# Kernel optimization log

Measured on AMD Instinct MI355X. Metric: run time of the kernel, lower is better.

The kernel has to match this reference:

```python
import jax, jax.numpy as jnp
import numpy as np
import math

D_MODEL = 1024
N_HEADS = 16
HEAD_DIM = D_MODEL // N_HEADS
SEQ_LEN = 8192
INCLUDE_LOCAL = 2


def get_dilated_positions(seq_len, include_local=2):
    # Faithful numpy port of the torch pattern generator (runs once at setup).
    max_attend = include_local + int(math.ceil(math.log2(seq_len + 1)))
    positions = np.zeros((seq_len, max_attend), dtype=np.int64)
    mask = np.zeros((seq_len, max_attend), dtype=bool)
    for i in range(seq_len):
        ap = [i]
        for j in range(1, include_local + 1):
            if i - j >= 0:
                ap.append(i - j)
        k = 2
        while i - 2 ** k >= 0:
            ap.append(i - 2 ** k)
            k += 1
        positions[i, :len(ap)] = ap
        mask[i, :len(ap)] = True
    return positions, mask


def setup_inputs() -> dict:
    key = jax.random.key(0)
    kx, kq, kk, kv, ko = jax.random.split(key, 5)
    x = jax.random.normal(kx, (1, SEQ_LEN, D_MODEL), dtype=jnp.float32)
    # nn.Linear(bias=False) weights, torch layout [out_features, in_features]
    s = 0.02
    q_w = jax.random.normal(kq, (D_MODEL, D_MODEL), dtype=jnp.float32) * s
    k_w = jax.random.normal(kk, (D_MODEL, D_MODEL), dtype=jnp.float32) * s
    v_w = jax.random.normal(kv, (D_MODEL, D_MODEL), dtype=jnp.float32) * s
    o_w = jax.random.normal(ko, (D_MODEL, D_MODEL), dtype=jnp.float32) * s
    pos_np, mask_np = get_dilated_positions(SEQ_LEN, INCLUDE_LOCAL)
    return {
        "x": x,
        "q_w": q_w, "k_w": k_w, "v_w": v_w, "o_w": o_w,
        "positions": jnp.asarray(pos_np),   # (S, A) int64 indices
        "attend_mask": jnp.asarray(mask_np) # (S, A) bool
    }


def reference(x, q_w, k_w, v_w, o_w, positions, attend_mask):
    B, S, _ = x.shape
    H, Dh = N_HEADS, HEAD_DIM
    scale = Dh ** -0.5

    q = (x @ q_w.T).reshape(B, S, H, Dh).transpose(0, 2, 1, 3)  # (B,H,S,Dh)
    k = (x @ k_w.T).reshape(B, S, H, Dh).transpose(0, 2, 1, 3)
    v = (x @ v_w.T).reshape(B, S, H, Dh).transpose(0, 2, 1, 3)

    # Gather K/V at the dilated positions: (B,H,S,A,Dh)
    k_sparse = k[:, :, positions, :]
    v_sparse = v[:, :, positions, :]

    scores = jnp.einsum('bhsd,bhsad->bhsa', q, k_sparse) * scale
    scores = jnp.where(attend_mask[None, None, :, :], scores, -jnp.inf)
    attn = jax.nn.softmax(scores, axis=-1)  # dropout p in eval / 0.0 -> identity

    out = jnp.einsum('bhsa,bhsad->bhsd', attn, v_sparse)
    out = out.transpose(0, 2, 1, 3).reshape(B, S, D_MODEL)
    return out @ o_w.T
```

## Files before the change

kernel.cpp:

```cpp
#include <hip/hip_runtime.h>
#include <hip/hip_bf16.h>

typedef __bf16 bf16_t;
typedef __bf16 bf16x4 __attribute__((ext_vector_type(4)));
typedef __bf16 bf16x8 __attribute__((ext_vector_type(8)));
typedef float floatx16 __attribute__((ext_vector_type(16)));

#define SEQ    8192
#define DM     1024
#define NHEADS 16
#define HDIM   64

__device__ __forceinline__ void async_ld16(bf16_t* lds, const bf16_t* g) {
  __builtin_amdgcn_global_load_lds(
      (__attribute__((address_space(1))) void*)g,
      (__attribute__((address_space(3))) void*)lds, 16, 0, 0);
}

__global__ __launch_bounds__(256)
void cvt_all(const float* __restrict__ x,  const float* __restrict__ qw,
             const float* __restrict__ kw, const float* __restrict__ vw,
             const float* __restrict__ ow,
             bf16_t* __restrict__ Xb,  bf16_t* __restrict__ QWb,
             bf16_t* __restrict__ KWb, bf16_t* __restrict__ VWb,
             bf16_t* __restrict__ OWb) {
  const int b = blockIdx.x;
  const float* in; bf16_t* out; int g;
  if (b < 8192) { in = x; out = Xb; g = b; }
  else {
    const int w  = (b - 8192) >> 10;
    const int wb = (b - 8192) & 1023;
    switch (w) {
      case 0:  in = qw; out = QWb; break;
      case 1:  in = kw; out = KWb; break;
      case 2:  in = vw; out = VWb; break;
      default: in = ow; out = OWb; break;
    }
    g = wb;
  }
  const int idx = (g * 256 + threadIdx.x) * 4;
  float4 v = *(const float4*)(in + idx);
  bf16x4 o = { (bf16_t)v.x, (bf16_t)v.y, (bf16_t)v.z, (bf16_t)v.w };
  *(bf16x4*)(out + idx) = o;
}

__global__ __launch_bounds__(256)
void gemm_qkv(const bf16_t* __restrict__ A,
              const bf16_t* __restrict__ Bq, const bf16_t* __restrict__ Bk,
              const bf16_t* __restrict__ Bv,
              bf16_t* __restrict__ Cq, bf16_t* __restrict__ Ck, bf16_t* __restrict__ Cv)
{
  const bf16_t* B = (blockIdx.z == 0) ? Bq : (blockIdx.z == 1) ? Bk : Bv;
  bf16_t*       C = (blockIdx.z == 0) ? Cq : (blockIdx.z == 1) ? Ck : Cv;
  constexpr int Kdim = DM;
  __shared__ __attribute__((aligned(16))) bf16_t sA[128 * 64];
  __shared__ __attribute__((aligned(16))) bf16_t sB[128 * 64];

  const int tid  = threadIdx.x;
  const int wave = tid >> 6;
  const int lane = tid & 63;
  const int l31  = lane & 31;
  const int half = lane >> 5;
  const int wr   = (wave >> 1) * 64;
  const int wc   = (wave & 1) * 64;

  const int gc = (lane & 7) ^ ((lane >> 3) & 7);
  const size_t arow0 = (size_t)blockIdx.x * 128 + wave * 32 + (lane >> 3);
  const size_t brow0 = (size_t)blockIdx.y * 128 + wave * 32 + (lane >> 3);
  const bf16_t* Ag = A + arow0 * Kdim + gc * 8;
  const bf16_t* Bg = B + brow0 * Kdim + gc * 8;
  bf16_t* sAw = sA + wave * 32 * 64;
  bf16_t* sBw = sB + wave * 32 * 64;

  floatx16 acc[2][2];
  #pragma unroll
  for (int i = 0; i < 2; ++i)
    #pragma unroll
    for (int j = 0; j < 2; ++j)
      acc[i][j] = (floatx16)(0.0f);

  const int sw = l31 & 7;

  for (int ko = 0; ko < Kdim; ko += 64) {
    #pragma unroll
    for (int n = 0; n < 4; ++n) {
      async_ld16(sAw + n * 512, Ag + (size_t)n * 8 * Kdim + ko);
      async_ld16(sBw + n * 512, Bg + (size_t)n * 8 * Kdim + ko);
    }
    __syncthreads();

    #pragma unroll
    for (int s = 0; s < 4; ++s) {
      const int ck   = s * 2 + half;
      const int slot = (ck ^ sw) * 8;
      bf16x8 af[2], bfr[2];
      #pragma unroll
      for (int mi = 0; mi < 2; ++mi)
        af[mi] = *(const bf16x8*)&sA[(wr + mi * 32 + l31) * 64 + slot];
      #pragma unroll
      for (int ni = 0; ni < 2; ++ni)
        bfr[ni] = *(const bf16x8*)&sB[(wc + ni * 32 + l31) * 64 + slot];

      #pragma unroll
      for (int mi = 0; mi < 2; ++mi)
        #pragma unroll
        for (int ni = 0; ni < 2; ++ni)
          acc[mi][ni] = __builtin_amdgcn_mfma_f32_32x32x16_bf16(af[mi], bfr[ni], acc[mi][ni], 0, 0, 0);
    }

    __syncthreads();
  }

  const float scl = (blockIdx.z == 0) ? 0.125f : 1.0f;
  const int crow0 = blockIdx.x * 128 + wr + 4 * half;
  const int ccol0 = blockIdx.y * 128 + wc + l31;
  #pragma unroll
  for (int mi = 0; mi < 2; ++mi)
    #pragma unroll
    for (int ni = 0; ni < 2; ++ni)
      #pragma unroll
      for (int r = 0; r < 16; ++r) {
        const int row = crow0 + mi * 32 + (r & 3) + 8 * (r >> 2);
        C[(size_t)row * DM + (ccol0 + ni * 32)] = (bf16_t)(acc[mi][ni][r] * scl);
      }
}

__global__ __launch_bounds__(256)
void gemm_out(const bf16_t* __restrict__ A, const bf16_t* __restrict__ B,
              float* __restrict__ C)
{
  constexpr int Kdim = DM;
  __shared__ __attribute__((aligned(16))) bf16_t sA[128 * 64];
  __shared__ __attribute__((aligned(16))) bf16_t sB[128 * 64];

  const int tid  = threadIdx.x;
  const int wave = tid >> 6;
  const int lane = tid & 63;
  const int l31  = lane & 31;
  const int half = lane >> 5;
  const int wr   = (wave >> 1) * 64;
  const int wc   = (wave & 1) * 64;

  const int gc = (lane & 7) ^ ((lane >> 3) & 7);
  const size_t arow0 = (size_t)blockIdx.x * 128 + wave * 32 + (lane >> 3);
  const size_t brow0 = (size_t)blockIdx.y * 128 + wave * 32 + (lane >> 3);
  const bf16_t* Ag = A + arow0 * Kdim + gc * 8;
  const bf16_t* Bg = B + brow0 * Kdim + gc * 8;
  bf16_t* sAw = sA + wave * 32 * 64;
  bf16_t* sBw = sB + wave * 32 * 64;

  floatx16 acc[2][2];
  #pragma unroll
  for (int i = 0; i < 2; ++i)
    #pragma unroll
    for (int j = 0; j < 2; ++j)
      acc[i][j] = (floatx16)(0.0f);

  const int sw = l31 & 7;

  for (int ko = 0; ko < Kdim; ko += 64) {
    #pragma unroll
    for (int n = 0; n < 4; ++n) {
      async_ld16(sAw + n * 512, Ag + (size_t)n * 8 * Kdim + ko);
      async_ld16(sBw + n * 512, Bg + (size_t)n * 8 * Kdim + ko);
    }
    __syncthreads();

    #pragma unroll
    for (int s = 0; s < 4; ++s) {
      const int ck   = s * 2 + half;
      const int slot = (ck ^ sw) * 8;
      bf16x8 af[2], bfr[2];
      #pragma unroll
      for (int mi = 0; mi < 2; ++mi)
        af[mi] = *(const bf16x8*)&sA[(wr + mi * 32 + l31) * 64 + slot];
      #pragma unroll
      for (int ni = 0; ni < 2; ++ni)
        bfr[ni] = *(const bf16x8*)&sB[(wc + ni * 32 + l31) * 64 + slot];

      #pragma unroll
      for (int mi = 0; mi < 2; ++mi)
        #pragma unroll
        for (int ni = 0; ni < 2; ++ni)
          acc[mi][ni] = __builtin_amdgcn_mfma_f32_32x32x16_bf16(af[mi], bfr[ni], acc[mi][ni], 0, 0, 0);
    }

    __syncthreads();
  }

  const int crow0 = blockIdx.x * 128 + wr + 4 * half;
  const int ccol0 = blockIdx.y * 128 + wc + l31;
  #pragma unroll
  for (int mi = 0; mi < 2; ++mi)
    #pragma unroll
    for (int ni = 0; ni < 2; ++ni)
      #pragma unroll
      for (int r = 0; r < 16; ++r) {
        const int row = crow0 + mi * 32 + (r & 3) + 8 * (r >> 2);
        C[(size_t)row * DM + (ccol0 + ni * 32)] = acc[mi][ni][r];
      }
}

__global__ __launch_bounds__(256)
void dilated_attn(const bf16_t* __restrict__ Q, const bf16_t* __restrict__ K,
                  const bf16_t* __restrict__ V, bf16_t* O)
{
  __shared__ float sM[2][64];
  __shared__ float sL[2][64];
  __shared__ float sAcc[2][64][17];

  const int lane = threadIdx.x & 63;
  const int wv   = threadIdx.x >> 6;
  const int ql   = wv >> 1;
  const int sub  = wv & 1;
  const int qb   = (blockIdx.x & 7) * 512 + (blockIdx.x >> 3);
  const int i    = qb * 2 + ql;
  const size_t base = (size_t)i * DM + lane * 16;

  bf16x8 q0 = *(const bf16x8*)(Q + base);
  bf16x8 q1 = *(const bf16x8*)(Q + base + 8);
  float qf[16];
  #pragma unroll
  for (int j = 0; j < 8; ++j) { qf[j] = (float)q0[j]; qf[j + 8] = (float)q1[j]; }

  const int npos = (i == 0) ? 1 : (33 - __builtin_clz((unsigned)i));
  auto pos_addr = [&](int t) -> size_t {
    const int off = (t == 0) ? 0 : (1 << (t - 1));
    return (size_t)(i - off) * DM + lane * 16;
  };

  float m = -INFINITY, l = 0.0f;
  float acc[16];
  #pragma unroll
  for (int j = 0; j < 16; ++j) acc[j] = 0.0f;

  int t = sub;
  if (t < npos) {
    size_t a = pos_addr(t);
    bf16x8 k0 = *(const bf16x8*)(K + a), k1 = *(const bf16x8*)(K + a + 8);
    bf16x8 v0 = *(const bf16x8*)(V + a), v1 = *(const bf16x8*)(V + a + 8);
    while (true) {
      const int tn = t + 2;
      const bool more = (tn < npos);
      bf16x8 nk0, nk1, nv0, nv1;
      if (more) {
        const size_t na = pos_addr(tn);
        nk0 = *(const bf16x8*)(K + na); nk1 = *(const bf16x8*)(K + na + 8);
        nv0 = *(const bf16x8*)(V + na); nv1 = *(const bf16x8*)(V + na + 8);
      }

      float sc = 0.0f;
      #pragma unroll
      for (int j = 0; j < 8; ++j) sc += qf[j] * (float)k0[j] + qf[j + 8] * (float)k1[j];
      sc += __shfl_xor(sc, 1, 64);
      sc += __shfl_xor(sc, 2, 64);

      float mn = fmaxf(m, sc);
      float co = __expf(m - mn);
      float w  = __expf(sc - mn);
      l = l * co + w;
      m = mn;
      #pragma unroll
      for (int j = 0; j < 8; ++j) {
        acc[j]     = acc[j]     * co + w * (float)v0[j];
        acc[j + 8] = acc[j + 8] * co + w * (float)v1[j];
      }

      if (!more) break;
      k0 = nk0; k1 = nk1; v0 = nv0; v1 = nv1;
      t = tn;
    }
  }

  if (sub == 1) {
    sM[ql][lane] = m;
    sL[ql][lane] = l;
    #pragma unroll
    for (int j = 0; j < 16; ++j) sAcc[ql][lane][j] = acc[j];
  }
  __syncthreads();
  if (sub == 0) {
    const float mb = sM[ql][lane], lb = sL[ql][lane];
    const float mt = fmaxf(m, mb);
    const float ca = __expf(m - mt);
    const float cb = __expf(mb - mt);
    const float inv = 1.0f / (l * ca + lb * cb);
    bf16x8 o0, o1;
    #pragma unroll
    for (int j = 0; j < 8; ++j) {
      o0[j] = (bf16_t)((acc[j]     * ca + sAcc[ql][lane][j]     * cb) * inv);
      o1[j] = (bf16_t)((acc[j + 8] * ca + sAcc[ql][lane][j + 8] * cb) * inv);
    }
    *(bf16x8*)(O + base)     = o0;
    *(bf16x8*)(O + base + 8) = o1;
  }
}

extern "C" void kernel_launch(void* const* d_in, const int* in_sizes, int n_in,
                              void* d_out, int out_size, void* d_ws, size_t ws_size,
                              hipStream_t stream) {
  (void)in_sizes; (void)n_in; (void)out_size; (void)ws_size;
  const float* x  = (const float*)d_in[0];
  const float* qw = (const float*)d_in[1];
  const float* kw = (const float*)d_in[2];
  const float* vw = (const float*)d_in[3];
  const float* ow = (const float*)d_in[4];
  float* out = (float*)d_out;

  bf16_t* Xb  = (bf16_t*)d_ws;
  bf16_t* Qb  = Xb  + (size_t)SEQ * DM;
  bf16_t* Kb  = Qb  + (size_t)SEQ * DM;
  bf16_t* Vb  = Kb  + (size_t)SEQ * DM;
  bf16_t* QWb = Vb  + (size_t)SEQ * DM;
  bf16_t* KWb = QWb + (size_t)DM * DM;
  bf16_t* VWb = KWb + (size_t)DM * DM;
  bf16_t* OWb = VWb + (size_t)DM * DM;
  bf16_t* AO  = Qb;

  cvt_all<<<dim3(8192 + 4096), dim3(256), 0, stream>>>(x, qw, kw, vw, ow,
                                                       Xb, QWb, KWb, VWb, OWb);

  gemm_qkv<<<dim3(SEQ / 128, DM / 128, 3), dim3(256), 0, stream>>>(Xb, QWb, KWb, VWb, Qb, Kb, Vb);
  dilated_attn<<<dim3(SEQ / 2), dim3(256), 0, stream>>>(Qb, Kb, Vb, AO);
  gemm_out<<<dim3(SEQ / 128, DM / 128), dim3(256), 0, stream>>>(AO, OWb, out);
}
```

Measured before the change: 213.7 us.

## Double-buffer projection GEMM, split QKV launches, and simplify attention to one wave per query

The QKV projection GEMM gains double-buffered LDS staging, so async global-to-LDS loads of the next K tile overlap MFMA work on the current one. The single fused QKV launch with a blockIdx.z select becomes three separate launches. The attention kernel now gives each wave one full query instead of splitting positions across two waves, which removes the LDS merge and the __syncthreads. The cost is twice the LDS per GEMM block, which may lower occupancy, extra launch overhead, and longer serial per-wave loops in attention.

```diff
diff --git a/kernel.cpp b/kernel.cpp
--- a/kernel.cpp
+++ b/kernel.cpp
@@ -44,17 +44,14 @@
   *(bf16x4*)(out + idx) = o;
 }
 
+
 __global__ __launch_bounds__(256)
-void gemm_qkv(const bf16_t* __restrict__ A,
-              const bf16_t* __restrict__ Bq, const bf16_t* __restrict__ Bk,
-              const bf16_t* __restrict__ Bv,
-              bf16_t* __restrict__ Cq, bf16_t* __restrict__ Ck, bf16_t* __restrict__ Cv)
+void gemm_proj(const bf16_t* __restrict__ A, const bf16_t* __restrict__ B,
+               bf16_t* __restrict__ C, float scl)
 {
-  const bf16_t* B = (blockIdx.z == 0) ? Bq : (blockIdx.z == 1) ? Bk : Bv;
-  bf16_t*       C = (blockIdx.z == 0) ? Cq : (blockIdx.z == 1) ? Ck : Cv;
   constexpr int Kdim = DM;
-  __shared__ __attribute__((aligned(16))) bf16_t sA[128 * 64];
-  __shared__ __attribute__((aligned(16))) bf16_t sB[128 * 64];
+  __shared__ __attribute__((aligned(16))) bf16_t sA[2][128 * 64];
+  __shared__ __attribute__((aligned(16))) bf16_t sB[2][128 * 64];
 
   const int tid  = threadIdx.x;
   const int wave = tid >> 6;
@@ -69,8 +66,6 @@
   const size_t brow0 = (size_t)blockIdx.y * 128 + wave * 32 + (lane >> 3);
   const bf16_t* Ag = A + arow0 * Kdim + gc * 8;
   const bf16_t* Bg = B + brow0 * Kdim + gc * 8;
-  bf16_t* sAw = sA + wave * 32 * 64;
-  bf16_t* sBw = sB + wave * 32 * 64;
 
   floatx16 acc[2][2];
   #pragma unroll
@@ -81,14 +76,14 @@
 
   const int sw = l31 & 7;
 
-  for (int ko = 0; ko < Kdim; ko += 64) {
+  auto stage = [&](int buf, int ko) {
     #pragma unroll
     for (int n = 0; n < 4; ++n) {
-      async_ld16(sAw + n * 512, Ag + (size_t)n * 8 * Kdim + ko);
-      async_ld16(sBw + n * 512, Bg + (size_t)n * 8 * Kdim + ko);
-    }
-    __syncthreads();
-
+      async_ld16(&sA[buf][(wave * 32 + n * 8) * 64], Ag + (size_t)n * 8 * Kdim + ko);
+      async_ld16(&sB[buf][(wave * 32 + n * 8) * 64], Bg + (size_t)n * 8 * Kdim + ko);
+    }
+  };
+  auto compute = [&](int buf) {
     #pragma unroll
     for (int s = 0; s < 4; ++s) {
       const int ck   = s * 2 + half;
@@ -96,22 +91,30 @@
       bf16x8 af[2], bfr[2];
       #pragma unroll
       for (int mi = 0; mi < 2; ++mi)
-        af[mi] = *(const bf16x8*)&sA[(wr + mi * 32 + l31) * 64 + slot];
+        af[mi] = *(const bf16x8*)&sA[buf][(wr + mi * 32 + l31) * 64 + slot];
       #pragma unroll
       for (int ni = 0; ni < 2; ++ni)
-        bfr[ni] = *(const bf16x8*)&sB[(wc + ni * 32 + l31) * 64 + slot];
-
+        bfr[ni] = *(const bf16x8*)&sB[buf][(wc + ni * 32 + l31) * 64 + slot];
       #pragma unroll
       for (int mi = 0; mi < 2; ++mi)
         #pragma unroll
         for (int ni = 0; ni < 2; ++ni)
           acc[mi][ni] = __builtin_amdgcn_mfma_f32_32x32x16_bf16(af[mi], bfr[ni], acc[mi][ni], 0, 0, 0);
     }
-
+  };
+
+  stage(0, 0);
+  __syncthreads();
+  for (int kp = 0; kp < 8; ++kp) {
+    const int ko = kp * 128;
+    stage(1, ko + 64);
+    compute(0);
     __syncthreads();
-  }
-
-  const float scl = (blockIdx.z == 0) ? 0.125f : 1.0f;
+    if (ko + 128 < Kdim) stage(0, ko + 128);
+    compute(1);
+    __syncthreads();
+  }
+
   const int crow0 = blockIdx.x * 128 + wr + 4 * half;
   const int ccol0 = blockIdx.y * 128 + wc + l31;
   #pragma unroll
@@ -126,8 +129,8 @@
 }
 
 __global__ __launch_bounds__(256)
-void gemm_out(const bf16_t* __restrict__ A, const bf16_t* __restrict__ B,
-              float* __restrict__ C)
+void gemm_outk(const bf16_t* __restrict__ A, const bf16_t* __restrict__ B,
+               float* __restrict__ C)
 {
   constexpr int Kdim = DM;
   __shared__ __attribute__((aligned(16))) bf16_t sA[128 * 64];
@@ -205,16 +208,10 @@
 void dilated_attn(const bf16_t* __restrict__ Q, const bf16_t* __restrict__ K,
                   const bf16_t* __restrict__ V, bf16_t* O)
 {
-  __shared__ float sM[2][64];
-  __shared__ float sL[2][64];
-  __shared__ float sAcc[2][64][17];
-
   const int lane = threadIdx.x & 63;
   const int wv   = threadIdx.x >> 6;
-  const int ql   = wv >> 1;
-  const int sub  = wv & 1;
-  const int qb   = (blockIdx.x & 7) * 512 + (blockIdx.x >> 3);
-  const int i    = qb * 2 + ql;
+  const int bid  = blockIdx.x;
+  const int i    = ((bid & 7) * 256 + (bid >> 3)) * 4 + wv;
   const size_t base = (size_t)i * DM + lane * 16;
 
   bf16x8 q0 = *(const bf16x8*)(Q + base);
@@ -234,13 +231,13 @@
   #pragma unroll
   for (int j = 0; j < 16; ++j) acc[j] = 0.0f;
 
-  int t = sub;
-  if (t < npos) {
-    size_t a = pos_addr(t);
+  {
+    size_t a = base;
     bf16x8 k0 = *(const bf16x8*)(K + a), k1 = *(const bf16x8*)(K + a + 8);
     bf16x8 v0 = *(const bf16x8*)(V + a), v1 = *(const bf16x8*)(V + a + 8);
+    int t = 0;
     while (true) {
-      const int tn = t + 2;
+      const int tn = t + 1;
       const bool more = (tn < npos);
       bf16x8 nk0, nk1, nv0, nv1;
       if (more) {
@@ -272,28 +269,15 @@
     }
   }
 
-  if (sub == 1) {
-    sM[ql][lane] = m;
-    sL[ql][lane] = l;
-    #pragma unroll
-    for (int j = 0; j < 16; ++j) sAcc[ql][lane][j] = acc[j];
-  }
-  __syncthreads();
-  if (sub == 0) {
-    const float mb = sM[ql][lane], lb = sL[ql][lane];
-    const float mt = fmaxf(m, mb);
-    const float ca = __expf(m - mt);
-    const float cb = __expf(mb - mt);
-    const float inv = 1.0f / (l * ca + lb * cb);
-    bf16x8 o0, o1;
-    #pragma unroll
-    for (int j = 0; j < 8; ++j) {
-      o0[j] = (bf16_t)((acc[j]     * ca + sAcc[ql][lane][j]     * cb) * inv);
-      o1[j] = (bf16_t)((acc[j + 8] * ca + sAcc[ql][lane][j + 8] * cb) * inv);
-    }
-    *(bf16x8*)(O + base)     = o0;
-    *(bf16x8*)(O + base + 8) = o1;
-  }
+  const float inv = 1.0f / l;
+  bf16x8 o0, o1;
+  #pragma unroll
+  for (int j = 0; j < 8; ++j) {
+    o0[j] = (bf16_t)(acc[j]     * inv);
+    o1[j] = (bf16_t)(acc[j + 8] * inv);
+  }
+  *(bf16x8*)(O + base)     = o0;
+  *(bf16x8*)(O + base + 8) = o1;
 }
 
 extern "C" void kernel_launch(void* const* d_in, const int* in_sizes, int n_in,
@@ -320,7 +304,10 @@
   cvt_all<<<dim3(8192 + 4096), dim3(256), 0, stream>>>(x, qw, kw, vw, ow,
                                                        Xb, QWb, KWb, VWb, OWb);
 
-  gemm_qkv<<<dim3(SEQ / 128, DM / 128, 3), dim3(256), 0, stream>>>(Xb, QWb, KWb, VWb, Qb, Kb, Vb);
-  dilated_attn<<<dim3(SEQ / 2), dim3(256), 0, stream>>>(Qb, Kb, Vb, AO);
-  gemm_out<<<dim3(SEQ / 128, DM / 128), dim3(256), 0, stream>>>(AO, OWb, out);
-}
+  dim3 pg(SEQ / 128, DM / 128);
+  gemm_proj<<<pg, dim3(256), 0, stream>>>(Xb, QWb, Qb, 0.125f);
+  gemm_proj<<<pg, dim3(256), 0, stream>>>(Xb, KWb, Kb, 1.0f);
+  gemm_proj<<<pg, dim3(256), 0, stream>>>(Xb, VWb, Vb, 1.0f);
+  dilated_attn<<<dim3(SEQ / 4), dim3(256), 0, stream>>>(Qb, Kb, Vb, AO);
+  gemm_outk<<<pg, dim3(256), 0, stream>>>(AO, OWb, out);
+}
```

Measured after the change: 240.8 us. 12.7% more time.
